# Kernel tuning notes

Hardware: AMD Instinct MI355X
Metric: run time of the kernel (lower is better)

## Reference

```python
import jax, jax.numpy as jnp
import numpy as np

B, L, D = 4, 2048, 1024
H, DH = 16, 64  # heads, head dim (D = H*DH)


def setup_inputs() -> dict:
    key = jax.random.key(0)
    k1, k2, k3 = jax.random.split(key, 3)
    scale = D ** -0.5
    xin = jax.random.normal(k1, (B, L, D), dtype=jnp.float32)
    W_qkv = jax.random.normal(k2, (D, 3 * D), dtype=jnp.float32) * scale
    W_o = jax.random.normal(k3, (D, D), dtype=jnp.float32) * scale
    return {"xin": xin, "W_qkv": W_qkv, "W_o": W_o}


def reference(xin, W_qkv, W_o):
    b, Lq, _ = xin.shape
    # QKV projection: (b, L, 3D). NOTE: original torch code reshapes the
    # (b, L, 3D) buffer directly to (b, 3, H, L, DH) — a non-standard axis
    # interleave — which we replicate faithfully.
    QKV = (xin @ W_qkv).reshape(b, 3, H, Lq, DH)
    Q, K, V = QKV[:, 0], QKV[:, 1], QKV[:, 2]  # each (b, H, L, DH)
    scores = jnp.einsum("bhqd,bhkd->bhqk", Q, K) * (DH ** -0.5)
    attn = jax.nn.softmax(scores, axis=-1)  # dropout_prob=0.0 -> identity
    out = jnp.einsum("bhqk,bhkd->bhqd", attn, V)
    out = out.transpose(0, 2, 1, 3).reshape(b, Lq, H * DH)
    return out @ W_o
```

## Files before the change

### kernel.cpp

```cpp
#include <hip/hip_runtime.h>
#include <stdint.h>

typedef short short8 __attribute__((ext_vector_type(8)));
typedef short short4v __attribute__((ext_vector_type(4)));
typedef float f32x4 __attribute__((ext_vector_type(4)));

#define LOG2E 1.44269504088896f
#define AS1 __attribute__((address_space(1)))
#define AS3 __attribute__((address_space(3)))

__device__ __forceinline__ float fexp2(float x) {
#if __has_builtin(__builtin_amdgcn_exp2f)
    return __builtin_amdgcn_exp2f(x);
#else
    return exp2f(x);
#endif
}
__device__ __forceinline__ unsigned short f2bfbits(float f) {
    unsigned x = __builtin_bit_cast(unsigned, f);
    unsigned r = x + 0x7fffu + ((x >> 16) & 1u);
    return (unsigned short)(r >> 16);
}
__device__ __forceinline__ float bfbits2f(unsigned short b) {
    unsigned u = ((unsigned)b) << 16;
    return __builtin_bit_cast(float, u);
}
__device__ __forceinline__ void unpack8(uint4 u, float4& f0, float4& f1) {
    f0.x = bfbits2f((unsigned short)(u.x & 0xffffu)); f0.y = bfbits2f((unsigned short)(u.x >> 16));
    f0.z = bfbits2f((unsigned short)(u.y & 0xffffu)); f0.w = bfbits2f((unsigned short)(u.y >> 16));
    f1.x = bfbits2f((unsigned short)(u.z & 0xffffu)); f1.y = bfbits2f((unsigned short)(u.z >> 16));
    f1.z = bfbits2f((unsigned short)(u.w & 0xffffu)); f1.w = bfbits2f((unsigned short)(u.w >> 16));
}
__device__ __forceinline__ unsigned pack2(float a, float b) {
    return (unsigned)f2bfbits(a) | ((unsigned)f2bfbits(b) << 16);
}
__device__ __forceinline__ unsigned pack2t(float a, float b) {
    unsigned ba = __builtin_bit_cast(unsigned, a);
    unsigned bb = __builtin_bit_cast(unsigned, b);
    return (ba >> 16) | (bb & 0xffff0000u);
}
__device__ __forceinline__ f32x4 mfma16(short4v a, short4v b, f32x4 c) {
#if __has_builtin(__builtin_amdgcn_mfma_f32_16x16x16bf16_1k)
    return __builtin_amdgcn_mfma_f32_16x16x16bf16_1k(a, b, c, 0, 0, 0);
#else
    asm("v_mfma_f32_16x16x16_bf16 %0, %1, %2, %0" : "+v"(c) : "v"(a), "v"(b));
    return c;
#endif
}
__device__ __forceinline__ void glds16(const void* gp, void* lp) {
    __builtin_amdgcn_global_load_lds((const AS1 unsigned*)(uintptr_t)gp,
                                     (AS3 unsigned*)(unsigned)(uintptr_t)lp, 16, 0, 0);
}

__global__ __launch_bounds__(256) void xbf_k(const float* __restrict__ x,
                                             unsigned short* __restrict__ y) {
    int i = (blockIdx.x * 256 + threadIdx.x) * 4;
    float4 v = *(const float4*)(x + i);
    uint2 u;
    u.x = pack2(v.x, v.y);
    u.y = pack2(v.z, v.w);
    *(uint2*)(y + i) = u;
}

__global__ __launch_bounds__(256) void t32cvt_k(const float* __restrict__ src,
                                                unsigned short* __restrict__ dst,
                                                int R, int C) {
    __shared__ float tile[32][36];
    int t = threadIdx.x;
    int bx = blockIdx.x, by = blockIdx.y;
    int r = t >> 3, c0 = (t & 7) * 4;
    *(float4*)&tile[r][c0] = *(const float4*)(src + (size_t)(by * 32 + r) * C + bx * 32 + c0);
    __syncthreads();
    uint2 u;
    u.x = pack2(tile[c0 + 0][r], tile[c0 + 1][r]);
    u.y = pack2(tile[c0 + 2][r], tile[c0 + 3][r]);
    *(uint2*)(dst + (size_t)(bx * 32 + r) * R + by * 32 + c0) = u;
}

template <bool CF32>
__global__ __launch_bounds__(256) void gemm_k(const unsigned short* __restrict__ A,
                                              const unsigned short* __restrict__ Bt,
                                              void* __restrict__ Cv,
                                              int M, int N, int K) {
    __shared__ unsigned short sA[128 * 32];
    __shared__ unsigned short sB[128 * 32];
    int t = threadIdx.x;
    int wid = t >> 6, lane = t & 63;
    int wm = (wid >> 1) * 64, wn = (wid & 1) * 64;
    int lm = lane & 15, lq = lane >> 4;
    int nwg = gridDim.x * gridDim.y;
    int orig = blockIdx.y * gridDim.x + blockIdx.x;
    int swz = (orig & 7) * (nwg >> 3) + (orig >> 3);
    int bxi = swz % gridDim.x, byi = swz / gridDim.x;
    size_t m0 = (size_t)byi * 128, n0 = (size_t)bxi * 128;
    int srow = t >> 2, scol = (t & 3) * 8;
    const unsigned short* ga0 = A + (m0 + srow) * K + scol;
    const unsigned short* ga1 = A + (m0 + 64 + srow) * K + scol;
    const unsigned short* gb0 = Bt + (n0 + srow) * K + scol;
    const unsigned short* gb1 = Bt + (n0 + 64 + srow) * K + scol;
    unsigned short* laA0 = &sA[wid * 512];
    unsigned short* laA1 = &sA[2048 + wid * 512];
    unsigned short* laB0 = &sB[wid * 512];
    unsigned short* laB1 = &sB[2048 + wid * 512];
    f32x4 acc[4][4] = {};
    for (int k0 = 0; k0 < K; k0 += 32) {
        __syncthreads();
        glds16(ga0 + k0, laA0);
        glds16(ga1 + k0, laA1);
        glds16(gb0 + k0, laB0);
        glds16(gb1 + k0, laB1);
        __syncthreads();
        short8 af[4], bfr[4];
        #pragma unroll
        for (int i = 0; i < 4; ++i) af[i] = *(const short8*)&sA[(wm + i * 16 + lm) * 32 + lq * 8];
        #pragma unroll
        for (int j = 0; j < 4; ++j) bfr[j] = *(const short8*)&sB[(wn + j * 16 + lm) * 32 + lq * 8];
        #pragma unroll
        for (int i = 0; i < 4; ++i)
            #pragma unroll
            for (int j = 0; j < 4; ++j)
                acc[i][j] = __builtin_amdgcn_mfma_f32_16x16x32_bf16(af[i], bfr[j], acc[i][j], 0, 0, 0);
    }
    #pragma unroll
    for (int i = 0; i < 4; ++i)
        #pragma unroll
        for (int j = 0; j < 4; ++j)
            #pragma unroll
            for (int r = 0; r < 4; ++r) {
                size_t row = m0 + wm + i * 16 + lq * 4 + r;
                size_t col = n0 + wn + j * 16 + lm;
                if (CF32) ((float*)Cv)[row * N + col] = acc[i][j][r];
                else ((unsigned short*)Cv)[row * N + col] = f2bfbits(acc[i][j][r]);
            }
}

__global__ __launch_bounds__(256) void vt_k(const unsigned short* __restrict__ qkv,
                                            unsigned short* __restrict__ vt) {
    __shared__ unsigned short tile[64 * 72];
    int kt = blockIdx.x, bh = blockIdx.y;
    int b = bh >> 4, h = bh & 15;
    const unsigned short* Vp = qkv + (size_t)b * 6291456 + 4194304 + (size_t)h * 131072;
    int t = threadIdx.x;
    int row = t >> 2, cc = (t & 3) * 16;
    const unsigned short* src = Vp + (size_t)(kt * 64 + row) * 64 + cc;
    *(uint4*)&tile[row * 72 + cc] = *(const uint4*)src;
    *(uint4*)&tile[row * 72 + cc + 8] = *(const uint4*)(src + 8);
    __syncthreads();
    unsigned v[8];
    #pragma unroll
    for (int j = 0; j < 8; ++j) {
        unsigned short a = tile[(cc + 2 * j) * 72 + row];
        unsigned short bsh = tile[(cc + 2 * j + 1) * 72 + row];
        v[j] = (unsigned)a | ((unsigned)bsh << 16);
    }
    unsigned short* dst = vt + ((size_t)bh * 64 + row) * 2048 + kt * 64 + cc;
    *(uint4*)dst = make_uint4(v[0], v[1], v[2], v[3]);
    *(uint4*)(dst + 8) = make_uint4(v[4], v[5], v[6], v[7]);
}

__global__ __launch_bounds__(256, 4) void attn_mfma(const unsigned short* __restrict__ qkv,
                                                    const unsigned short* __restrict__ vt,
                                                    unsigned short* __restrict__ aout) {
    __shared__ unsigned short Ks[2][64 * 64];
    __shared__ unsigned short Vs[2][64 * 64];
    int bid0 = blockIdx.x;
    int bid = (bid0 & 7) * 128 + (bid0 >> 3);
    int qt = bid & 15, h = (bid >> 4) & 15, b = bid >> 8;
    int t = threadIdx.x;
    int wave = t >> 6, lane = t & 63, lm = lane & 15, quad = lane >> 4;
    const unsigned short* Qb = qkv + (size_t)b * 6291456 + (size_t)h * 131072;
    const unsigned short* Kb = Qb + 2097152;
    const unsigned short* Vtb = vt + (size_t)(b * 16 + h) * 131072;
    int q0 = qt * 128 + wave * 32;

    const float qs = 0.125f * LOG2E;
    short8 qf[2][2];
    #pragma unroll
    for (int i = 0; i < 2; ++i)
        #pragma unroll
        for (int c = 0; c < 2; ++c) {
            uint4 u = *(const uint4*)(Qb + (size_t)(q0 + i * 16 + lm) * 64 + c * 32 + quad * 8);
            float4 f0, f1; unpack8(u, f0, f1);
            uint4 v;
            v.x = pack2(f0.x * qs, f0.y * qs);
            v.y = pack2(f0.z * qs, f0.w * qs);
            v.z = pack2(f1.x * qs, f1.y * qs);
            v.w = pack2(f1.z * qs, f1.w * qs);
            qf[i][c] = *(short8*)&v;
        }

    short4v ones4;
    #pragma unroll
    for (int z = 0; z < 4; ++z) ones4[z] = (short)0x3F80;

    f32x4 o[2][4] = {};
    f32x4 l_acc[2] = {};

    int srow = t >> 2, scolb = (t & 3) * 16;
    int ss = (srow & 7) << 3;
    int sc0 = srow * 64 + (scolb ^ ss);
    int sc1 = srow * 64 + ((scolb + 8) ^ ss);
    int rs = (lm & 7) << 3;

    uint4 k0r, k1r, v0r, v1r;
    {
        const unsigned short* kp = Kb + (size_t)srow * 64 + scolb;
        k0r = *(const uint4*)kp;
        k1r = *(const uint4*)(kp + 8);
        const unsigned short* vp = Vtb + (size_t)srow * 2048 + scolb;
        v0r = *(const uint4*)vp;
        v1r = *(const uint4*)(vp + 8);
        *(uint4*)&Ks[0][sc0] = k0r;
        *(uint4*)&Ks[0][sc1] = k1r;
        *(uint4*)&Vs[0][sc0] = v0r;
        *(uint4*)&Vs[0][sc1] = v1r;
    }

    #pragma unroll 1
    for (int kt = 0; kt < 32; ++kt) {
        __syncthreads();

        if (kt < 31) {
            const unsigned short* kp = Kb + (size_t)((kt + 1) * 64 + srow) * 64 + scolb;
            k0r = *(const uint4*)kp;
            k1r = *(const uint4*)(kp + 8);
            const unsigned short* vp = Vtb + (size_t)srow * 2048 + (kt + 1) * 64 + scolb;
            v0r = *(const uint4*)vp;
            v1r = *(const uint4*)(vp + 8);
        }

        const unsigned short* ks = Ks[kt & 1];
        const unsigned short* vs = Vs[kt & 1];
        __builtin_amdgcn_s_setprio(1);

        short4v pf[2][4];
        #pragma unroll
        for (int j = 0; j < 4; ++j) {
            short8 kf0 = *(const short8*)&ks[(j * 16 + lm) * 64 + ((quad * 8) ^ rs)];
            short8 kf1 = *(const short8*)&ks[(j * 16 + lm) * 64 + ((32 + quad * 8) ^ rs)];
            #pragma unroll
            for (int i = 0; i < 2; ++i) {
                f32x4 sf = {0.f, 0.f, 0.f, 0.f};
                sf = __builtin_amdgcn_mfma_f32_16x16x32_bf16(kf0, qf[i][0], sf, 0, 0, 0);
                sf = __builtin_amdgcn_mfma_f32_16x16x32_bf16(kf1, qf[i][1], sf, 0, 0, 0);
                uint2 u;
                u.x = pack2t(fexp2(sf[0]), fexp2(sf[1]));
                u.y = pack2t(fexp2(sf[2]), fexp2(sf[3]));
                pf[i][j] = *(short4v*)&u;
            }
        }

        #pragma unroll
        for (int jd = 0; jd < 4; ++jd)
            #pragma unroll
            for (int j = 0; j < 4; ++j) {
                short4v vf = *(const short4v*)&vs[(jd * 16 + lm) * 64 + ((j * 16 + quad * 4) ^ rs)];
                o[0][jd] = mfma16(pf[0][j], vf, o[0][jd]);
                o[1][jd] = mfma16(pf[1][j], vf, o[1][jd]);
            }
        #pragma unroll
        for (int j = 0; j < 4; ++j) {
            l_acc[0] = mfma16(pf[0][j], ones4, l_acc[0]);
            l_acc[1] = mfma16(pf[1][j], ones4, l_acc[1]);
        }
        __builtin_amdgcn_s_setprio(0);

        if (kt < 31) {
            unsigned short* kd = Ks[(kt + 1) & 1];
            unsigned short* vd = Vs[(kt + 1) & 1];
            *(uint4*)&kd[sc0] = k0r;
            *(uint4*)&kd[sc1] = k1r;
            *(uint4*)&vd[sc0] = v0r;
            *(uint4*)&vd[sc1] = v1r;
        }
    }
    #pragma unroll
    for (int i = 0; i < 2; ++i)
        #pragma unroll
        for (int r = 0; r < 4; ++r) {
            float inv = 1.f / l_acc[i][r];
            int q = q0 + i * 16 + quad * 4 + r;
            size_t rowbase = ((size_t)b * 2048 + q) * 1024 + h * 64;
            #pragma unroll
            for (int jd = 0; jd < 4; ++jd)
                aout[rowbase + jd * 16 + lm] = f2bfbits(o[i][jd][r] * inv);
        }
}

extern "C" void kernel_launch(void* const* d_in, const int* in_sizes, int n_in,
                              void* d_out, int out_size, void* d_ws, size_t ws_size,
                              hipStream_t stream) {
    const float* xin  = (const float*)d_in[0];
    const float* wqkv = (const float*)d_in[1];
    const float* wo   = (const float*)d_in[2];
    float* out = (float*)d_out;

    char* ws = (char*)d_ws;
    unsigned short* qkv   = (unsigned short*)(ws);
    unsigned short* attn  = (unsigned short*)(ws + 50331648);
    unsigned short* wqkvT = (unsigned short*)(ws + 67108864);
    unsigned short* woT   = (unsigned short*)(ws + 73400320);
    unsigned short* vt    = (unsigned short*)(ws + 75497472);
    unsigned short* xb    = (unsigned short*)(ws + 92274688);

    dim3 blk(256);
    xbf_k<<<dim3(8192), blk, 0, stream>>>(xin, xb);
    t32cvt_k<<<dim3(3072 / 32, 1024 / 32), blk, 0, stream>>>(wqkv, wqkvT, 1024, 3072);
    t32cvt_k<<<dim3(1024 / 32, 1024 / 32), blk, 0, stream>>>(wo, woT, 1024, 1024);
    gemm_k<false><<<dim3(3072 / 128, 8192 / 128), blk, 0, stream>>>(xb, wqkvT, qkv, 8192, 3072, 1024);
    vt_k<<<dim3(32, 64), blk, 0, stream>>>(qkv, vt);
    attn_mfma<<<dim3(1024), blk, 0, stream>>>(qkv, vt, attn);
    gemm_k<true><<<dim3(1024 / 128, 8192 / 128), blk, 0, stream>>>(attn, woT, out, 8192, 1024, 1024);
}
```

Before: 284.8 us.

## Split attention KV range across two wave groups and merge partials in LDS

The attention kernel now launches 512 threads per block, split into two groups of four waves. Each group processes half of the key/value sequence for the same 128 query rows, with its own double-buffered LDS region. The partial O and row sums from group 1 are then reduced through shared memory into group 0, which writes the output. This halves the serial KV loop length per block to expose more parallelism and latency hiding, at the cost of doubling LDS use to 64KB per block and adding a reduction step. Merging by plain addition is valid only because the kernel uses no running max in its softmax.

```diff
diff --git a/kernel.cpp b/kernel.cpp
--- a/kernel.cpp
+++ b/kernel.cpp
@@ -158,20 +158,24 @@
     *(uint4*)(dst + 8) = make_uint4(v[4], v[5], v[6], v[7]);
 }
 
-__global__ __launch_bounds__(256, 4) void attn_mfma(const unsigned short* __restrict__ qkv,
+__global__ __launch_bounds__(512, 2) void attn_mfma(const unsigned short* __restrict__ qkv,
                                                     const unsigned short* __restrict__ vt,
                                                     unsigned short* __restrict__ aout) {
-    __shared__ unsigned short Ks[2][64 * 64];
-    __shared__ unsigned short Vs[2][64 * 64];
+    __shared__ __align__(16) char smem[65536];
     int bid0 = blockIdx.x;
     int bid = (bid0 & 7) * 128 + (bid0 >> 3);
     int qt = bid & 15, h = (bid >> 4) & 15, b = bid >> 8;
     int t = threadIdx.x;
     int wave = t >> 6, lane = t & 63, lm = lane & 15, quad = lane >> 4;
+    int g = wave >> 2;
+    int qw = wave & 3;
     const unsigned short* Qb = qkv + (size_t)b * 6291456 + (size_t)h * 131072;
     const unsigned short* Kb = Qb + 2097152;
     const unsigned short* Vtb = vt + (size_t)(b * 16 + h) * 131072;
-    int q0 = qt * 128 + wave * 32;
+    int q0 = qt * 128 + qw * 32;
+    int kbase = g * 16;
+
+    unsigned short* gb = (unsigned short*)(smem + g * 32768);
 
     const float qs = 0.125f * LOG2E;
     short8 qf[2][2];
@@ -196,7 +200,8 @@
     f32x4 o[2][4] = {};
     f32x4 l_acc[2] = {};
 
-    int srow = t >> 2, scolb = (t & 3) * 16;
+    int tg = t & 255;
+    int srow = tg >> 2, scolb = (tg & 3) * 16;
     int ss = (srow & 7) << 3;
     int sc0 = srow * 64 + (scolb ^ ss);
     int sc1 = srow * 64 + ((scolb + 8) ^ ss);
@@ -204,33 +209,33 @@
 
     uint4 k0r, k1r, v0r, v1r;
     {
-        const unsigned short* kp = Kb + (size_t)srow * 64 + scolb;
+        const unsigned short* kp = Kb + (size_t)(kbase * 64 + srow) * 64 + scolb;
         k0r = *(const uint4*)kp;
         k1r = *(const uint4*)(kp + 8);
-        const unsigned short* vp = Vtb + (size_t)srow * 2048 + scolb;
+        const unsigned short* vp = Vtb + (size_t)srow * 2048 + kbase * 64 + scolb;
         v0r = *(const uint4*)vp;
         v1r = *(const uint4*)(vp + 8);
-        *(uint4*)&Ks[0][sc0] = k0r;
-        *(uint4*)&Ks[0][sc1] = k1r;
-        *(uint4*)&Vs[0][sc0] = v0r;
-        *(uint4*)&Vs[0][sc1] = v1r;
+        *(uint4*)&gb[sc0] = k0r;
+        *(uint4*)&gb[sc1] = k1r;
+        *(uint4*)&gb[8192 + sc0] = v0r;
+        *(uint4*)&gb[8192 + sc1] = v1r;
     }
 
     #pragma unroll 1
-    for (int kt = 0; kt < 32; ++kt) {
+    for (int kt = 0; kt < 16; ++kt) {
         __syncthreads();
 
-        if (kt < 31) {
-            const unsigned short* kp = Kb + (size_t)((kt + 1) * 64 + srow) * 64 + scolb;
+        if (kt < 15) {
+            const unsigned short* kp = Kb + (size_t)((kbase + kt + 1) * 64 + srow) * 64 + scolb;
             k0r = *(const uint4*)kp;
             k1r = *(const uint4*)(kp + 8);
-            const unsigned short* vp = Vtb + (size_t)srow * 2048 + (kt + 1) * 64 + scolb;
+            const unsigned short* vp = Vtb + (size_t)srow * 2048 + (kbase + kt + 1) * 64 + scolb;
             v0r = *(const uint4*)vp;
             v1r = *(const uint4*)(vp + 8);
         }
 
-        const unsigned short* ks = Ks[kt & 1];
-        const unsigned short* vs = Vs[kt & 1];
+        const unsigned short* ks = gb + (kt & 1) * 4096;
+        const unsigned short* vs = gb + 8192 + (kt & 1) * 4096;
         __builtin_amdgcn_s_setprio(1);
 
         short4v pf[2][4];
@@ -265,26 +270,48 @@
         }
         __builtin_amdgcn_s_setprio(0);
 
-        if (kt < 31) {
-            unsigned short* kd = Ks[(kt + 1) & 1];
-            unsigned short* vd = Vs[(kt + 1) & 1];
+        if (kt < 15) {
+            unsigned short* kd = gb + ((kt + 1) & 1) * 4096;
+            unsigned short* vd = gb + 8192 + ((kt + 1) & 1) * 4096;
             *(uint4*)&kd[sc0] = k0r;
             *(uint4*)&kd[sc1] = k1r;
             *(uint4*)&vd[sc0] = v0r;
             *(uint4*)&vd[sc1] = v1r;
         }
     }
-    #pragma unroll
-    for (int i = 0; i < 2; ++i)
-        #pragma unroll
-        for (int r = 0; r < 4; ++r) {
-            float inv = 1.f / l_acc[i][r];
-            int q = q0 + i * 16 + quad * 4 + r;
-            size_t rowbase = ((size_t)b * 2048 + q) * 1024 + h * 64;
-            #pragma unroll
-            for (int jd = 0; jd < 4; ++jd)
-                aout[rowbase + jd * 16 + lm] = f2bfbits(o[i][jd][r] * inv);
-        }
+
+    __syncthreads();
+    float* Ol = (float*)smem;
+    float* Ll = (float*)(smem + 32768);
+    if (g == 1) {
+        #pragma unroll
+        for (int i = 0; i < 2; ++i)
+            #pragma unroll
+            for (int r = 0; r < 4; ++r) {
+                int ql = qw * 32 + i * 16 + quad * 4 + r;
+                #pragma unroll
+                for (int jd = 0; jd < 4; ++jd)
+                    Ol[ql * 64 + jd * 16 + lm] = o[i][jd][r];
+                if (lm == 0) Ll[ql] = l_acc[i][r];
+            }
+    }
+    __syncthreads();
+    if (g == 0) {
+        #pragma unroll
+        for (int i = 0; i < 2; ++i)
+            #pragma unroll
+            for (int r = 0; r < 4; ++r) {
+                int ql = qw * 32 + i * 16 + quad * 4 + r;
+                float inv = 1.f / (l_acc[i][r] + Ll[ql]);
+                int q = qt * 128 + ql;
+                size_t rowbase = ((size_t)b * 2048 + q) * 1024 + h * 64;
+                #pragma unroll
+                for (int jd = 0; jd < 4; ++jd) {
+                    float val = (o[i][jd][r] + Ol[ql * 64 + jd * 16 + lm]) * inv;
+                    aout[rowbase + jd * 16 + lm] = f2bfbits(val);
+                }
+            }
+    }
 }
 
 extern "C" void kernel_launch(void* const* d_in, const int* in_sizes, int n_in,
@@ -309,6 +336,6 @@
     t32cvt_k<<<dim3(1024 / 32, 1024 / 32), blk, 0, stream>>>(wo, woT, 1024, 1024);
     gemm_k<false><<<dim3(3072 / 128, 8192 / 128), blk, 0, stream>>>(xb, wqkvT, qkv, 8192, 3072, 1024);
     vt_k<<<dim3(32, 64), blk, 0, stream>>>(qkv, vt);
-    attn_mfma<<<dim3(1024), blk, 0, stream>>>(qkv, vt, attn);
+    attn_mfma<<<dim3(1024), dim3(512), 0, stream>>>(qkv, vt, attn);
     gemm_k<true><<<dim3(1024 / 128, 8192 / 128), blk, 0, stream>>>(attn, woT, out, 8192, 1024, 1024);
 }
```

Result: slower. 315.5 us (+10.8%).
